# Kernel tuning notes

Hardware: AMD Instinct MI355X
Metric: run time of the kernel (lower is better)

Reference implementation:

```python
import jax, jax.numpy as jnp
import numpy as np

N = 524288
E = 16          # embedding_dim
R = 128         # dense grid resolution
H = 128         # hidden_dim
W0_SIREN = 30.0


def trilinear(grid, p):
    """grid: [R,R,R,E]; p: [N,3] in [0,1]. Returns [N,E]."""
    r = grid.shape[0]
    x = p * (r - 1)
    i0 = jnp.clip(jnp.floor(x), 0, r - 2).astype(jnp.int32)   # [N,3]
    f = x - i0.astype(x.dtype)                                # [N,3] fractional
    gf = grid.reshape(-1, grid.shape[-1])                     # [R^3, E]
    out = jnp.zeros((p.shape[0], grid.shape[-1]), dtype=grid.dtype)
    for dx in (0, 1):
        wx = f[:, 0] if dx else (1.0 - f[:, 0])
        for dy in (0, 1):
            wy = f[:, 1] if dy else (1.0 - f[:, 1])
            for dz in (0, 1):
                wz = f[:, 2] if dz else (1.0 - f[:, 2])
                idx = (i0[:, 0] + dx) * r * r + (i0[:, 1] + dy) * r + (i0[:, 2] + dz)
                out = out + gf[idx] * (wx * wy * wz)[:, None]
    return out


def siren(h, W0, b0, W1, b1, Wo, bo):
    h = jnp.sin(W0_SIREN * (h @ W0.T + b0))
    h = jnp.sin(W0_SIREN * (h @ W1.T + b1))
    return h @ Wo.T + bo   # [N,1]


def setup_inputs() -> dict:
    key = jax.random.key(0)
    ks = jax.random.split(key, 8)
    positions = jax.random.uniform(ks[0], (N, 3), dtype=jnp.float32)  # in [0,1)
    grid = jax.random.uniform(ks[1], (R, R, R, E), jnp.float32, -1e-4, 1e-4)
    din = E + 3
    c0 = float(np.sqrt(6.0 / din) / W0_SIREN)
    c1 = float(np.sqrt(6.0 / H) / W0_SIREN)
    W0 = jax.random.uniform(ks[2], (H, din), jnp.float32, -c0, c0)
    b0 = jax.random.uniform(ks[3], (H,), jnp.float32, -c0, c0)
    W1 = jax.random.uniform(ks[4], (H, H), jnp.float32, -c1, c1)
    b1 = jax.random.uniform(ks[5], (H,), jnp.float32, -c1, c1)
    Wo = jax.random.uniform(ks[6], (1, H), jnp.float32, -c1, c1)
    bo = jax.random.uniform(ks[7], (1,), jnp.float32, -c1, c1)
    return {"positions": positions, "grid": grid, "W0": W0, "b0": b0,
            "W1": W1, "b1": b1, "Wo": Wo, "bo": bo}


def reference(positions, grid, W0, b0, W1, b1, Wo, bo):
    # torch code rebinds positions = positions*0.5+0.5 BEFORE autograd.grad,
    # so the eikonal gradient is w.r.t. the transformed coordinates p.
    p = positions * 0.5 + 0.5

    def sdf_fn(pp):
        emb = trilinear(grid, pp)
        return siren(jnp.concatenate([emb, pp], axis=-1), W0, b0, W1, b1, Wo, bo)

    sdf, vjp_fn = jax.vjp(sdf_fn, p)
    (grad_x,) = vjp_fn(jnp.ones_like(sdf))
    return sdf, grad_x
```

## Files before the change

kernel.cpp:

```cpp
#include <hip/hip_runtime.h>
#include <math.h>

#define NPTS 524288
#define EDIM 16
#define RES  128
#define HDIM 128
#define DIN  19
#define OXs  (RES*RES*EDIM)
#define OYs  (RES*EDIM)
#define OZs  (EDIM)
#define NBLK 256
#define NITER (NPTS / (NBLK * 128))

typedef _Float16 f16;
typedef __attribute__((ext_vector_type(8))) _Float16 f16x8;
typedef __attribute__((ext_vector_type(4))) float f32x4;

#define WS_P1 0
#define WS_P2 32768
#define WS_P0 65536
#define WS_P3 73728
#define WS_T  81920
#define WS_BYTES 84992

__global__ void pack_weights(const float* __restrict__ W0, const float* __restrict__ b0,
                             const float* __restrict__ W1, const float* __restrict__ b1,
                             const float* __restrict__ Wo, unsigned char* __restrict__ ws) {
    int idx = blockIdx.x * 256 + threadIdx.x;
    f16* p1 = (f16*)(ws + WS_P1);
    f16* p2 = (f16*)(ws + WS_P2);
    f16* p0 = (f16*)(ws + WS_P0);
    f16* p3 = (f16*)(ws + WS_P3);
    float* tb = (float*)(ws + WS_T);
    if (idx < 16384) {
        int e = idx & 7, l = (idx >> 3) & 63, t = (idx >> 9) & 3, nt = idx >> 11;
        int c = l & 15, g = l >> 4;
        p1[idx] = (f16)W1[(c + 16*nt)*HDIM + (8*g + e + 32*t)];
    } else if (idx < 32768) {
        int i = idx - 16384;
        int e = i & 7, l = (i >> 3) & 63, t = (i >> 9) & 3, nt = i >> 11;
        int c = l & 15, g = l >> 4;
        p2[i] = (f16)W1[(8*g + e + 32*t)*HDIM + (c + 16*nt)];
    } else if (idx < 36864) {
        int i = idx - 32768;
        int e = i & 7, l = (i >> 3) & 63, nt = i >> 9;
        int c = l & 15, g = l >> 4;
        int d = 8*g + e;
        p0[i] = (d < EDIM) ? (f16)W0[(c + 16*nt)*DIN + d] : (f16)0.f;
    } else if (idx < 40960) {
        int i = idx - 36864;
        int e = i & 7, l = (i >> 3) & 63, t = (i >> 9) & 3, nt = i >> 11;
        int c = l & 15, g = l >> 4;
        int din = c + 16*nt;
        p3[i] = (din < DIN) ? (f16)W0[(8*g + e + 32*t)*DIN + din] : (f16)0.f;
    } else if (idx < 41728) {
        int i = idx - 40960;
        int j = i & 127, sel = i >> 7;
        float v;
        if (sel == 0)      v = W0[j*DIN + 16];
        else if (sel == 1) v = W0[j*DIN + 17];
        else if (sel == 2) v = W0[j*DIN + 18];
        else if (sel == 3) v = b0[j];
        else if (sel == 4) v = b1[j];
        else               v = Wo[j];
        tb[i] = v;
    }
}

__global__ __launch_bounds__(512, 2)
void sdf_mfma(const float* __restrict__ pos,
              const float* __restrict__ gridp,
              const unsigned char* __restrict__ ws,
              const float* __restrict__ bo,
              float* __restrict__ out) {
    __shared__ f16 sP1[16384];
    __shared__ f16 sP2[16384];
    __shared__ f16 sP0[4096];
    __shared__ f16 sP3[4096];
    __shared__ float sT[768];
    __shared__ unsigned char sBounce[8][4352];

    const int tid = threadIdx.x;
    {
        const uint4* src = (const uint4*)ws;
        uint4* d1 = (uint4*)sP1;
        uint4* d2 = (uint4*)sP2;
        uint4* d0 = (uint4*)sP0;
        uint4* d3 = (uint4*)sP3;
        uint4* dt = (uint4*)sT;
        d1[tid]        = src[tid];
        d1[tid + 512]  = src[tid + 512];
        d1[tid + 1024] = src[tid + 1024];
        d1[tid + 1536] = src[tid + 1536];
        d2[tid]        = src[2048 + tid];
        d2[tid + 512]  = src[2560 + tid];
        d2[tid + 1024] = src[3072 + tid];
        d2[tid + 1536] = src[3584 + tid];
        d0[tid] = src[4096 + tid];
        d3[tid] = src[4608 + tid];
        if (tid < 192) dt[tid] = src[5120 + tid];
    }
    __syncthreads();

    const int l = tid & 63, w = tid >> 6;
    const int c = l & 15, g = l >> 4;

    f16* sBW = (f16*)sBounce[w];
    const f16x8* P0 = (const f16x8*)sP0;
    const f16x8* P1 = (const f16x8*)sP1;
    const f16x8* P2 = (const f16x8*)sP2;
    const f16x8* P3 = (const f16x8*)sP3;
    const f32x4 z4 = {0.f, 0.f, 0.f, 0.f};
    const float bov = bo[0];

#pragma unroll 1
    for (int it = 0; it < NITER; ++it) {
        const int pbase = (blockIdx.x * NITER + it) * 128 + w * 16;
        const int pt = pbase + c;

        const float px = fmaf(pos[3*pt+0], 0.5f, 0.5f);
        const float py = fmaf(pos[3*pt+1], 0.5f, 0.5f);
        const float pz = fmaf(pos[3*pt+2], 0.5f, 0.5f);
        const float x0 = px*127.f, x1 = py*127.f, x2 = pz*127.f;
        int i0 = (int)floorf(x0); i0 = i0 < 0 ? 0 : (i0 > 126 ? 126 : i0);
        int i1 = (int)floorf(x1); i1 = i1 < 0 ? 0 : (i1 > 126 ? 126 : i1);
        int i2 = (int)floorf(x2); i2 = i2 < 0 ? 0 : (i2 > 126 ? 126 : i2);
        const float f0 = x0 - (float)i0, f1 = x1 - (float)i1, f2 = x2 - (float)i2;
        const float wx1 = f0, wx0 = 1.f - f0;
        const float wy1 = f1, wy0 = 1.f - f1;
        const float wz1 = f2, wz0 = 1.f - f2;
        const float* gb = gridp + (size_t)((i0*RES + i1)*RES + i2)*EDIM;

        float w8[8] = {0.f,0.f,0.f,0.f,0.f,0.f,0.f,0.f};
        if (g < 2) {
#pragma unroll
            for (int cr = 0; cr < 8; ++cr) {
                const float* gp = gb + ((cr>>2)&1)*OXs + ((cr>>1)&1)*OYs + (cr&1)*OZs + 8*g;
                float4 qa = *(const float4*)gp;
                float4 qb = *(const float4*)(gp + 4);
                const float wc = ((cr&4)?wx1:wx0) * ((cr&2)?wy1:wy0) * ((cr&1)?wz1:wz0);
                w8[0] = fmaf(wc, qa.x, w8[0]);  w8[1] = fmaf(wc, qa.y, w8[1]);
                w8[2] = fmaf(wc, qa.z, w8[2]);  w8[3] = fmaf(wc, qa.w, w8[3]);
                w8[4] = fmaf(wc, qb.x, w8[4]);  w8[5] = fmaf(wc, qb.y, w8[5]);
                w8[6] = fmaf(wc, qb.z, w8[6]);  w8[7] = fmaf(wc, qb.w, w8[7]);
            }
        }
        f16x8 afe;
#pragma unroll
        for (int m = 0; m < 8; ++m) afe[m] = (f16)w8[m];

        f32x4 acc[8];
#pragma unroll
        for (int nt = 0; nt < 8; ++nt)
            acc[nt] = __builtin_amdgcn_mfma_f32_16x16x32_f16(afe, P0[nt*64 + l], z4, 0, 0, 0);

        float rpx[4], rpy[4], rpz[4];
#pragma unroll
        for (int r = 0; r < 4; ++r) {
            const int pr = pbase + 4*g + r;
            rpx[r] = fmaf(pos[3*pr+0], 0.5f, 0.5f);
            rpy[r] = fmaf(pos[3*pr+1], 0.5f, 0.5f);
            rpz[r] = fmaf(pos[3*pr+2], 0.5f, 0.5f);
        }
        float t0a[8][4];
#pragma unroll
        for (int nt = 0; nt < 8; ++nt) {
            const int j = c + 16*nt;
            const float t16 = sT[j], t17 = sT[128+j], t18 = sT[256+j], tb0 = sT[384+j];
#pragma unroll
            for (int r = 0; r < 4; ++r) {
                float a0 = acc[nt][r] + tb0;
                a0 = fmaf(rpx[r], t16, a0);
                a0 = fmaf(rpy[r], t17, a0);
                a0 = fmaf(rpz[r], t18, a0);
                const float t0 = 30.f * a0;
                t0a[nt][r] = t0;
                sBW[(4*g + r)*136 + j] = (f16)__sinf(t0);
            }
        }
        asm volatile("s_waitcnt lgkmcnt(0)" ::: "memory");

        f16x8 af[4];
#pragma unroll
        for (int t = 0; t < 4; ++t)
            af[t] = *(const f16x8*)&sBW[c*136 + 32*t + 8*g];
#pragma unroll
        for (int nt = 0; nt < 8; ++nt) {
            f32x4 a = z4;
#pragma unroll
            for (int t = 0; t < 4; ++t)
                a = __builtin_amdgcn_mfma_f32_16x16x32_f16(af[t], P1[(nt*4+t)*64 + l], a, 0, 0, 0);
            acc[nt] = a;
        }

        float sp[4] = {0.f, 0.f, 0.f, 0.f};
#pragma unroll
        for (int nt = 0; nt < 8; ++nt) {
            const int j = c + 16*nt;
            const float b1j = sT[512+j], woj = sT[640+j];
#pragma unroll
            for (int r = 0; r < 4; ++r) {
                const float t1 = 30.f * (acc[nt][r] + b1j);
                sp[r] = fmaf(woj, __sinf(t1), sp[r]);
                sBW[(4*g + r)*136 + j] = (f16)(30.f * woj * __cosf(t1));
            }
        }
#pragma unroll
        for (int r = 0; r < 4; ++r) {
            sp[r] += __shfl_xor(sp[r], 1);
            sp[r] += __shfl_xor(sp[r], 2);
            sp[r] += __shfl_xor(sp[r], 4);
            sp[r] += __shfl_xor(sp[r], 8);
        }
        if (c == 0) {
#pragma unroll
            for (int r = 0; r < 4; ++r) out[pbase + 4*g + r] = sp[r] + bov;
        }
        asm volatile("s_waitcnt lgkmcnt(0)" ::: "memory");

        float4 ca[2][4];
#pragma unroll
        for (int h = 0; h < 2; ++h) {
            const int cr = 2*g + h;
            const float* gp = gb + ((cr>>2)&1)*OXs + ((cr>>1)&1)*OYs + (cr&1)*OZs;
            ca[h][0] = *(const float4*)gp;
            ca[h][1] = *(const float4*)(gp + 4);
            ca[h][2] = *(const float4*)(gp + 8);
            ca[h][3] = *(const float4*)(gp + 12);
        }

#pragma unroll
        for (int t = 0; t < 4; ++t)
            af[t] = *(const f16x8*)&sBW[c*136 + 32*t + 8*g];
#pragma unroll
        for (int nt = 0; nt < 8; ++nt) {
            f32x4 a = z4;
#pragma unroll
            for (int t = 0; t < 4; ++t)
                a = __builtin_amdgcn_mfma_f32_16x16x32_f16(af[t], P2[(nt*4+t)*64 + l], a, 0, 0, 0);
            acc[nt] = a;
        }

#pragma unroll
        for (int nt = 0; nt < 8; ++nt) {
            const int k = c + 16*nt;
#pragma unroll
            for (int r = 0; r < 4; ++r) {
                const float da0 = acc[nt][r] * (30.f * __cosf(t0a[nt][r]));
                sBW[(4*g + r)*136 + k] = (f16)da0;
            }
        }
        asm volatile("s_waitcnt lgkmcnt(0)" ::: "memory");

#pragma unroll
        for (int t = 0; t < 4; ++t)
            af[t] = *(const f16x8*)&sBW[c*136 + 32*t + 8*g];
        f32x4 d3a = z4, d3b = z4;
#pragma unroll
        for (int t = 0; t < 4; ++t) {
            d3a = __builtin_amdgcn_mfma_f32_16x16x32_f16(af[t], P3[t*64 + l],     d3a, 0, 0, 0);
            d3b = __builtin_amdgcn_mfma_f32_16x16x32_f16(af[t], P3[(4+t)*64 + l], d3b, 0, 0, 0);
        }

        float* sDV = (float*)sBounce[w];
#pragma unroll
        for (int r = 0; r < 4; ++r) sDV[(4*g + r)*20 + c] = d3a[r];
        if (c < 3) {
#pragma unroll
            for (int r = 0; r < 4; ++r) sDV[(4*g + r)*20 + 16 + c] = d3b[r];
        }
        asm volatile("s_waitcnt lgkmcnt(0)" ::: "memory");

        const f32x4 dva = *(const f32x4*)&sDV[c*20 + 0];
        const f32x4 dvb = *(const f32x4*)&sDV[c*20 + 4];
        const f32x4 dvc = *(const f32x4*)&sDV[c*20 + 8];
        const f32x4 dvd = *(const f32x4*)&sDV[c*20 + 12];
        float scv[2];
#pragma unroll
        for (int h = 0; h < 2; ++h) {
            float s = ca[h][0].x*dva[0] + ca[h][0].y*dva[1] + ca[h][0].z*dva[2] + ca[h][0].w*dva[3]
                    + ca[h][1].x*dvb[0] + ca[h][1].y*dvb[1] + ca[h][1].z*dvb[2] + ca[h][1].w*dvb[3]
                    + ca[h][2].x*dvc[0] + ca[h][2].y*dvc[1] + ca[h][2].z*dvc[2] + ca[h][2].w*dvc[3]
                    + ca[h][3].x*dvd[0] + ca[h][3].y*dvd[1] + ca[h][3].z*dvd[2] + ca[h][3].w*dvd[3];
            scv[h] = s;
        }
        float* sSC = (float*)sBounce[w] + 320;
        sSC[c*8 + 2*g]     = scv[0];
        sSC[c*8 + 2*g + 1] = scv[1];
        asm volatile("s_waitcnt lgkmcnt(0)" ::: "memory");
        if (g == 0) {
            const float* scp = &sSC[c*8];
            const float sc0 = scp[0], sc1 = scp[1], sc2 = scp[2], sc3 = scp[3];
            const float sc4 = scp[4], sc5 = scp[5], sc6 = scp[6], sc7 = scp[7];
            const float gx = 127.f * (wy0*wz0*(sc4-sc0) + wy0*wz1*(sc5-sc1) +
                                      wy1*wz0*(sc6-sc2) + wy1*wz1*(sc7-sc3));
            const float gy = 127.f * (wx0*wz0*(sc2-sc0) + wx0*wz1*(sc3-sc1) +
                                      wx1*wz0*(sc6-sc4) + wx1*wz1*(sc7-sc5));
            const float gz = 127.f * (wx0*wy0*(sc1-sc0) + wx0*wy1*(sc3-sc2) +
                                      wx1*wy0*(sc5-sc4) + wx1*wy1*(sc7-sc6));
            out[NPTS + 3*pt + 0] = gx + sDV[c*20 + 16];
            out[NPTS + 3*pt + 1] = gy + sDV[c*20 + 17];
            out[NPTS + 3*pt + 2] = gz + sDV[c*20 + 18];
        }
    }
}

#define JCHUNK 64
__global__ void transpose_w1(const float* __restrict__ W1, float* __restrict__ W1T) {
    int idx = blockIdx.x * 256 + threadIdx.x;
    if (idx < HDIM * HDIM) {
        int j = idx >> 7, k = idx & 127;
        W1T[k * HDIM + j] = W1[j * HDIM + k];
    }
}
#define LOAD16(gq)                                   \
    float4 q0 = *(const float4*)((gq) + 0);          \
    float4 q1 = *(const float4*)((gq) + 4);          \
    float4 q2 = *(const float4*)((gq) + 8);          \
    float4 q3 = *(const float4*)((gq) + 12);

template<int RS, int CS>
__global__ __launch_bounds__(256, 2)
void sdf_fused(const float* __restrict__ pos, const float* __restrict__ gridp,
               const float* __restrict__ W0, const float* __restrict__ b0,
               const float* __restrict__ W1m, const float* __restrict__ b1,
               const float* __restrict__ Wo, const float* __restrict__ bo,
               float* __restrict__ out) {
    const int i = blockIdx.x * 256 + threadIdx.x;
    if (i >= NPTS) return;
    const float W0S = 30.0f;
    const float px = fmaf(pos[3*i+0], 0.5f, 0.5f);
    const float py = fmaf(pos[3*i+1], 0.5f, 0.5f);
    const float pz = fmaf(pos[3*i+2], 0.5f, 0.5f);
    const float x0 = px*127.f, x1 = py*127.f, x2 = pz*127.f;
    int i0 = (int)floorf(x0); i0 = i0 < 0 ? 0 : (i0 > 126 ? 126 : i0);
    int i1 = (int)floorf(x1); i1 = i1 < 0 ? 0 : (i1 > 126 ? 126 : i1);
    int i2 = (int)floorf(x2); i2 = i2 < 0 ? 0 : (i2 > 126 ? 126 : i2);
    const float f0 = x0-(float)i0, f1 = x1-(float)i1, f2 = x2-(float)i2;
    const float wx1 = f0, wx0 = 1.f-f0, wy1 = f1, wy0 = 1.f-f1, wz1 = f2, wz0 = 1.f-f2;
    const float* gb = gridp + (size_t)((i0*RES+i1)*RES+i2)*EDIM;
    float cw[8];
    cw[0]=wx0*wy0*wz0; cw[1]=wx0*wy0*wz1; cw[2]=wx0*wy1*wz0; cw[3]=wx0*wy1*wz1;
    cw[4]=wx1*wy0*wz0; cw[5]=wx1*wy0*wz1; cw[6]=wx1*wy1*wz0; cw[7]=wx1*wy1*wz1;
    float v[DIN];
#pragma unroll
    for (int e = 0; e < EDIM; ++e) v[e] = 0.f;
#pragma unroll
    for (int cr = 0; cr < 8; ++cr) {
        const float* gq = gb + ((cr>>2)&1)*OXs + ((cr>>1)&1)*OYs + (cr&1)*OZs;
        LOAD16(gq);
        const float wc = cw[cr];
        v[0]=fmaf(wc,q0.x,v[0]); v[1]=fmaf(wc,q0.y,v[1]); v[2]=fmaf(wc,q0.z,v[2]); v[3]=fmaf(wc,q0.w,v[3]);
        v[4]=fmaf(wc,q1.x,v[4]); v[5]=fmaf(wc,q1.y,v[5]); v[6]=fmaf(wc,q1.z,v[6]); v[7]=fmaf(wc,q1.w,v[7]);
        v[8]=fmaf(wc,q2.x,v[8]); v[9]=fmaf(wc,q2.y,v[9]); v[10]=fmaf(wc,q2.z,v[10]); v[11]=fmaf(wc,q2.w,v[11]);
        v[12]=fmaf(wc,q3.x,v[12]); v[13]=fmaf(wc,q3.y,v[13]); v[14]=fmaf(wc,q3.z,v[14]); v[15]=fmaf(wc,q3.w,v[15]);
    }
    v[16]=px; v[17]=py; v[18]=pz;
    float dv[DIN];
#pragma unroll
    for (int m = 0; m < DIN; ++m) dv[m] = 0.f;
    float sdf = bo[0];
#pragma unroll 1
    for (int cch = 0; cch < HDIM/JCHUNK; ++cch) {
        const int j0 = cch * JCHUNK;
        float a1c[JCHUNK];
#pragma unroll
        for (int jj = 0; jj < JCHUNK; ++jj) a1c[jj] = 0.f;
#pragma unroll 1
        for (int k = 0; k < HDIM; ++k) {
            float a0 = b0[k];
            const float* w0r = W0 + k*DIN;
#pragma unroll
            for (int m = 0; m < DIN; ++m) a0 = fmaf(w0r[m], v[m], a0);
            const float h1 = __sinf(W0S*a0);
            const float* wr = W1m + k*RS + j0*CS;
#pragma unroll
            for (int jj = 0; jj < JCHUNK; ++jj) a1c[jj] = fmaf(wr[jj*CS], h1, a1c[jj]);
        }
#pragma unroll
        for (int jj = 0; jj < JCHUNK; ++jj) {
            const float t = W0S*(a1c[jj] + b1[j0+jj]);
            float s, co; __sincosf(t, &s, &co);
            const float wo = Wo[j0+jj];
            sdf = fmaf(wo, s, sdf);
            a1c[jj] = (W0S*wo)*co;
        }
#pragma unroll 1
        for (int k = 0; k < HDIM; ++k) {
            const float* wr = W1m + k*RS + j0*CS;
            float s0=0.f,s1=0.f,s2=0.f,s3=0.f;
#pragma unroll
            for (int jj = 0; jj < JCHUNK; jj += 4) {
                s0 = fmaf(wr[(jj+0)*CS], a1c[jj+0], s0);
                s1 = fmaf(wr[(jj+1)*CS], a1c[jj+1], s1);
                s2 = fmaf(wr[(jj+2)*CS], a1c[jj+2], s2);
                s3 = fmaf(wr[(jj+3)*CS], a1c[jj+3], s3);
            }
            const float dh1 = (s0+s1)+(s2+s3);
            float a0 = b0[k];
            const float* w0r = W0 + k*DIN;
#pragma unroll
            for (int m = 0; m < DIN; ++m) a0 = fmaf(w0r[m], v[m], a0);
            const float da0 = dh1 * W0S * __cosf(W0S*a0);
#pragma unroll
            for (int m = 0; m < DIN; ++m) dv[m] = fmaf(w0r[m], da0, dv[m]);
        }
    }
    float sc[8];
#pragma unroll
    for (int cr = 0; cr < 8; ++cr) {
        const float* gq = gb + ((cr>>2)&1)*OXs + ((cr>>1)&1)*OYs + (cr&1)*OZs;
        LOAD16(gq);
        float t0 = q0.x*dv[0]+q0.y*dv[1]+q0.z*dv[2]+q0.w*dv[3];
        float t1 = q1.x*dv[4]+q1.y*dv[5]+q1.z*dv[6]+q1.w*dv[7];
        float t2 = q2.x*dv[8]+q2.y*dv[9]+q2.z*dv[10]+q2.w*dv[11];
        float t3 = q3.x*dv[12]+q3.y*dv[13]+q3.z*dv[14]+q3.w*dv[15];
        sc[cr] = (t0+t1)+(t2+t3);
    }
    const float gx = 127.f*(wy0*wz0*(sc[4]-sc[0]) + wy0*wz1*(sc[5]-sc[1]) + wy1*wz0*(sc[6]-sc[2]) + wy1*wz1*(sc[7]-sc[3]));
    const float gy = 127.f*(wx0*wz0*(sc[2]-sc[0]) + wx0*wz1*(sc[3]-sc[1]) + wx1*wz0*(sc[6]-sc[4]) + wx1*wz1*(sc[7]-sc[5]));
    const float gz = 127.f*(wx0*wy0*(sc[1]-sc[0]) + wx0*wy1*(sc[3]-sc[2]) + wx1*wy0*(sc[5]-sc[4]) + wx1*wy1*(sc[7]-sc[6]));
    out[i] = sdf;
    out[NPTS + 3*i + 0] = gx + dv[16];
    out[NPTS + 3*i + 1] = gy + dv[17];
    out[NPTS + 3*i + 2] = gz + dv[18];
}

extern "C" void kernel_launch(void* const* d_in, const int* in_sizes, int n_in,
                              void* d_out, int out_size, void* d_ws, size_t ws_size,
                              hipStream_t stream) {
    const float* pos  = (const float*)d_in[0];
    const float* grid = (const float*)d_in[1];
    const float* W0   = (const float*)d_in[2];
    const float* b0   = (const float*)d_in[3];
    const float* W1   = (const float*)d_in[4];
    const float* b1   = (const float*)d_in[5];
    const float* Wo   = (const float*)d_in[6];
    const float* bo   = (const float*)d_in[7];
    float* out = (float*)d_out;

    if (ws_size >= (size_t)WS_BYTES) {
        pack_weights<<<(41728 + 255)/256, 256, 0, stream>>>(W0, b0, W1, b1, Wo, (unsigned char*)d_ws);
        sdf_mfma<<<NBLK, 512, 0, stream>>>(pos, grid, (const unsigned char*)d_ws, bo, out);
    } else if (ws_size >= (size_t)(HDIM*HDIM*sizeof(float))) {
        float* W1T = (float*)d_ws;
        transpose_w1<<<(HDIM*HDIM + 255)/256, 256, 0, stream>>>(W1, W1T);
        sdf_fused<HDIM, 1><<<NPTS/256, 256, 0, stream>>>(pos, grid, W0, b0, W1T, b1, Wo, bo, out);
    } else {
        sdf_fused<1, HDIM><<<NPTS/256, 256, 0, stream>>>(pos, grid, W0, b0, W1, b1, Wo, bo, out);
    }
}
```

Measured before the change: 123.7 us.

## Process two 16-point batches per wave per iteration to interleave stages

Each wave now handles two independent 16-point tiles per loop iteration, with a separate LDS bounce buffer for each, and runs each stage (embedding+layer0, layer1, backward layer1, backward layer0/grid grads) for both tiles before the next wait. The point is to give the scheduler two independent MFMA/transcendental chains so gather and LDS latency are hidden, and to halve the number of waitcnt barriers per point. In exchange, register pressure rises (t0a doubles to 64 floats) under launch_bounds(512,2), LDS per block roughly doubles for the bounce buffers, and there is a risk of spills or lower occupancy.

```diff
diff --git a/kernel.cpp b/kernel.cpp
--- a/kernel.cpp
+++ b/kernel.cpp
@@ -10,7 +10,7 @@
 #define OYs  (RES*EDIM)
 #define OZs  (EDIM)
 #define NBLK 256
-#define NITER (NPTS / (NBLK * 128))
+#define NITER 8
 
 typedef _Float16 f16;
 typedef __attribute__((ext_vector_type(8))) _Float16 f16x8;
@@ -78,7 +78,7 @@
     __shared__ f16 sP0[4096];
     __shared__ f16 sP3[4096];
     __shared__ float sT[768];
-    __shared__ unsigned char sBounce[8][4352];
+    __shared__ unsigned char sBounce[8][2][4352];
 
     const int tid = threadIdx.x;
     {
@@ -105,7 +105,8 @@
     const int l = tid & 63, w = tid >> 6;
     const int c = l & 15, g = l >> 4;
 
-    f16* sBW = (f16*)sBounce[w];
+    f16* const sBW0 = (f16*)sBounce[w][0];
+    f16* const sBW1 = (f16*)sBounce[w][1];
     const f16x8* P0 = (const f16x8*)sP0;
     const f16x8* P1 = (const f16x8*)sP1;
     const f16x8* P2 = (const f16x8*)sP2;
@@ -115,192 +116,222 @@
 
 #pragma unroll 1
     for (int it = 0; it < NITER; ++it) {
-        const int pbase = (blockIdx.x * NITER + it) * 128 + w * 16;
-        const int pt = pbase + c;
-
-        const float px = fmaf(pos[3*pt+0], 0.5f, 0.5f);
-        const float py = fmaf(pos[3*pt+1], 0.5f, 0.5f);
-        const float pz = fmaf(pos[3*pt+2], 0.5f, 0.5f);
-        const float x0 = px*127.f, x1 = py*127.f, x2 = pz*127.f;
-        int i0 = (int)floorf(x0); i0 = i0 < 0 ? 0 : (i0 > 126 ? 126 : i0);
-        int i1 = (int)floorf(x1); i1 = i1 < 0 ? 0 : (i1 > 126 ? 126 : i1);
-        int i2 = (int)floorf(x2); i2 = i2 < 0 ? 0 : (i2 > 126 ? 126 : i2);
-        const float f0 = x0 - (float)i0, f1 = x1 - (float)i1, f2 = x2 - (float)i2;
-        const float wx1 = f0, wx0 = 1.f - f0;
-        const float wy1 = f1, wy0 = 1.f - f1;
-        const float wz1 = f2, wz0 = 1.f - f2;
-        const float* gb = gridp + (size_t)((i0*RES + i1)*RES + i2)*EDIM;
-
-        float w8[8] = {0.f,0.f,0.f,0.f,0.f,0.f,0.f,0.f};
-        if (g < 2) {
-#pragma unroll
-            for (int cr = 0; cr < 8; ++cr) {
-                const float* gp = gb + ((cr>>2)&1)*OXs + ((cr>>1)&1)*OYs + (cr&1)*OZs + 8*g;
-                float4 qa = *(const float4*)gp;
-                float4 qb = *(const float4*)(gp + 4);
-                const float wc = ((cr&4)?wx1:wx0) * ((cr&2)?wy1:wy0) * ((cr&1)?wz1:wz0);
-                w8[0] = fmaf(wc, qa.x, w8[0]);  w8[1] = fmaf(wc, qa.y, w8[1]);
-                w8[2] = fmaf(wc, qa.z, w8[2]);  w8[3] = fmaf(wc, qa.w, w8[3]);
-                w8[4] = fmaf(wc, qb.x, w8[4]);  w8[5] = fmaf(wc, qb.y, w8[5]);
-                w8[6] = fmaf(wc, qb.z, w8[6]);  w8[7] = fmaf(wc, qb.w, w8[7]);
-            }
-        }
-        f16x8 afe;
-#pragma unroll
-        for (int m = 0; m < 8; ++m) afe[m] = (f16)w8[m];
-
-        f32x4 acc[8];
-#pragma unroll
-        for (int nt = 0; nt < 8; ++nt)
-            acc[nt] = __builtin_amdgcn_mfma_f32_16x16x32_f16(afe, P0[nt*64 + l], z4, 0, 0, 0);
-
-        float rpx[4], rpy[4], rpz[4];
-#pragma unroll
-        for (int r = 0; r < 4; ++r) {
-            const int pr = pbase + 4*g + r;
-            rpx[r] = fmaf(pos[3*pr+0], 0.5f, 0.5f);
-            rpy[r] = fmaf(pos[3*pr+1], 0.5f, 0.5f);
-            rpz[r] = fmaf(pos[3*pr+2], 0.5f, 0.5f);
-        }
-        float t0a[8][4];
-#pragma unroll
-        for (int nt = 0; nt < 8; ++nt) {
-            const int j = c + 16*nt;
-            const float t16 = sT[j], t17 = sT[128+j], t18 = sT[256+j], tb0 = sT[384+j];
+        const int base = (blockIdx.x * NITER + it) * 256 + w * 32;
+
+        float t0a[2][8][4];
+        const float* gb[2];
+        float wx0[2], wx1[2], wy0[2], wy1[2], wz0[2], wz1[2];
+
+#pragma unroll
+        for (int b = 0; b < 2; ++b) {
+            f16* const sBW = b ? sBW1 : sBW0;
+            const int pbase = base + b * 16;
+            const int pt = pbase + c;
+
+            const float px = fmaf(pos[3*pt+0], 0.5f, 0.5f);
+            const float py = fmaf(pos[3*pt+1], 0.5f, 0.5f);
+            const float pz = fmaf(pos[3*pt+2], 0.5f, 0.5f);
+            const float x0 = px*127.f, x1 = py*127.f, x2 = pz*127.f;
+            int i0 = (int)floorf(x0); i0 = i0 < 0 ? 0 : (i0 > 126 ? 126 : i0);
+            int i1 = (int)floorf(x1); i1 = i1 < 0 ? 0 : (i1 > 126 ? 126 : i1);
+            int i2 = (int)floorf(x2); i2 = i2 < 0 ? 0 : (i2 > 126 ? 126 : i2);
+            const float f0 = x0 - (float)i0, f1 = x1 - (float)i1, f2 = x2 - (float)i2;
+            wx1[b] = f0; wx0[b] = 1.f - f0;
+            wy1[b] = f1; wy0[b] = 1.f - f1;
+            wz1[b] = f2; wz0[b] = 1.f - f2;
+            gb[b] = gridp + (size_t)((i0*RES + i1)*RES + i2)*EDIM;
+
+            float w8[8] = {0.f,0.f,0.f,0.f,0.f,0.f,0.f,0.f};
+            if (g < 2) {
+#pragma unroll
+                for (int cr = 0; cr < 8; ++cr) {
+                    const float* gp = gb[b] + ((cr>>2)&1)*OXs + ((cr>>1)&1)*OYs + (cr&1)*OZs + 8*g;
+                    float4 qa = *(const float4*)gp;
+                    float4 qb = *(const float4*)(gp + 4);
+                    const float wc = ((cr&4)?wx1[b]:wx0[b]) * ((cr&2)?wy1[b]:wy0[b]) * ((cr&1)?wz1[b]:wz0[b]);
+                    w8[0] = fmaf(wc, qa.x, w8[0]);  w8[1] = fmaf(wc, qa.y, w8[1]);
+                    w8[2] = fmaf(wc, qa.z, w8[2]);  w8[3] = fmaf(wc, qa.w, w8[3]);
+                    w8[4] = fmaf(wc, qb.x, w8[4]);  w8[5] = fmaf(wc, qb.y, w8[5]);
+                    w8[6] = fmaf(wc, qb.z, w8[6]);  w8[7] = fmaf(wc, qb.w, w8[7]);
+                }
+            }
+            f16x8 afe;
+#pragma unroll
+            for (int m = 0; m < 8; ++m) afe[m] = (f16)w8[m];
+
+            f32x4 acc[8];
+#pragma unroll
+            for (int nt = 0; nt < 8; ++nt)
+                acc[nt] = __builtin_amdgcn_mfma_f32_16x16x32_f16(afe, P0[nt*64 + l], z4, 0, 0, 0);
+
+            float rpx[4], rpy[4], rpz[4];
 #pragma unroll
             for (int r = 0; r < 4; ++r) {
-                float a0 = acc[nt][r] + tb0;
-                a0 = fmaf(rpx[r], t16, a0);
-                a0 = fmaf(rpy[r], t17, a0);
-                a0 = fmaf(rpz[r], t18, a0);
-                const float t0 = 30.f * a0;
-                t0a[nt][r] = t0;
-                sBW[(4*g + r)*136 + j] = (f16)__sinf(t0);
+                const int pr = pbase + 4*g + r;
+                rpx[r] = fmaf(pos[3*pr+0], 0.5f, 0.5f);
+                rpy[r] = fmaf(pos[3*pr+1], 0.5f, 0.5f);
+                rpz[r] = fmaf(pos[3*pr+2], 0.5f, 0.5f);
+            }
+#pragma unroll
+            for (int nt = 0; nt < 8; ++nt) {
+                const int j = c + 16*nt;
+                const float t16 = sT[j], t17 = sT[128+j], t18 = sT[256+j], tb0 = sT[384+j];
+#pragma unroll
+                for (int r = 0; r < 4; ++r) {
+                    float a0 = acc[nt][r] + tb0;
+                    a0 = fmaf(rpx[r], t16, a0);
+                    a0 = fmaf(rpy[r], t17, a0);
+                    a0 = fmaf(rpz[r], t18, a0);
+                    const float t0 = 30.f * a0;
+                    t0a[b][nt][r] = t0;
+                    sBW[(4*g + r)*136 + j] = (f16)__sinf(t0);
+                }
             }
         }
         asm volatile("s_waitcnt lgkmcnt(0)" ::: "memory");
 
-        f16x8 af[4];
-#pragma unroll
-        for (int t = 0; t < 4; ++t)
-            af[t] = *(const f16x8*)&sBW[c*136 + 32*t + 8*g];
-#pragma unroll
-        for (int nt = 0; nt < 8; ++nt) {
-            f32x4 a = z4;
+#pragma unroll
+        for (int b = 0; b < 2; ++b) {
+            f16* const sBW = b ? sBW1 : sBW0;
+            const int pbase = base + b * 16;
+
+            f16x8 af[4];
 #pragma unroll
             for (int t = 0; t < 4; ++t)
-                a = __builtin_amdgcn_mfma_f32_16x16x32_f16(af[t], P1[(nt*4+t)*64 + l], a, 0, 0, 0);
-            acc[nt] = a;
-        }
-
-        float sp[4] = {0.f, 0.f, 0.f, 0.f};
-#pragma unroll
-        for (int nt = 0; nt < 8; ++nt) {
-            const int j = c + 16*nt;
-            const float b1j = sT[512+j], woj = sT[640+j];
+                af[t] = *(const f16x8*)&sBW[c*136 + 32*t + 8*g];
+            f32x4 acc[8];
+#pragma unroll
+            for (int nt = 0; nt < 8; ++nt) {
+                f32x4 a = z4;
+#pragma unroll
+                for (int t = 0; t < 4; ++t)
+                    a = __builtin_amdgcn_mfma_f32_16x16x32_f16(af[t], P1[(nt*4+t)*64 + l], a, 0, 0, 0);
+                acc[nt] = a;
+            }
+
+            float sp[4] = {0.f, 0.f, 0.f, 0.f};
+#pragma unroll
+            for (int nt = 0; nt < 8; ++nt) {
+                const int j = c + 16*nt;
+                const float b1j = sT[512+j], woj = sT[640+j];
+#pragma unroll
+                for (int r = 0; r < 4; ++r) {
+                    const float t1 = 30.f * (acc[nt][r] + b1j);
+                    sp[r] = fmaf(woj, __sinf(t1), sp[r]);
+                    sBW[(4*g + r)*136 + j] = (f16)(30.f * woj * __cosf(t1));
+                }
+            }
 #pragma unroll
             for (int r = 0; r < 4; ++r) {
-                const float t1 = 30.f * (acc[nt][r] + b1j);
-                sp[r] = fmaf(woj, __sinf(t1), sp[r]);
-                sBW[(4*g + r)*136 + j] = (f16)(30.f * woj * __cosf(t1));
-            }
-        }
-#pragma unroll
-        for (int r = 0; r < 4; ++r) {
-            sp[r] += __shfl_xor(sp[r], 1);
-            sp[r] += __shfl_xor(sp[r], 2);
-            sp[r] += __shfl_xor(sp[r], 4);
-            sp[r] += __shfl_xor(sp[r], 8);
-        }
-        if (c == 0) {
-#pragma unroll
-            for (int r = 0; r < 4; ++r) out[pbase + 4*g + r] = sp[r] + bov;
+                sp[r] += __shfl_xor(sp[r], 1);
+                sp[r] += __shfl_xor(sp[r], 2);
+                sp[r] += __shfl_xor(sp[r], 4);
+                sp[r] += __shfl_xor(sp[r], 8);
+            }
+            if (c == 0) {
+#pragma unroll
+                for (int r = 0; r < 4; ++r) out[pbase + 4*g + r] = sp[r] + bov;
+            }
         }
         asm volatile("s_waitcnt lgkmcnt(0)" ::: "memory");
 
-        float4 ca[2][4];
-#pragma unroll
-        for (int h = 0; h < 2; ++h) {
-            const int cr = 2*g + h;
-            const float* gp = gb + ((cr>>2)&1)*OXs + ((cr>>1)&1)*OYs + (cr&1)*OZs;
-            ca[h][0] = *(const float4*)gp;
-            ca[h][1] = *(const float4*)(gp + 4);
-            ca[h][2] = *(const float4*)(gp + 8);
-            ca[h][3] = *(const float4*)(gp + 12);
-        }
-
-#pragma unroll
-        for (int t = 0; t < 4; ++t)
-            af[t] = *(const f16x8*)&sBW[c*136 + 32*t + 8*g];
-#pragma unroll
-        for (int nt = 0; nt < 8; ++nt) {
-            f32x4 a = z4;
+#pragma unroll
+        for (int b = 0; b < 2; ++b) {
+            f16* const sBW = b ? sBW1 : sBW0;
+
+            f16x8 af[4];
 #pragma unroll
             for (int t = 0; t < 4; ++t)
-                a = __builtin_amdgcn_mfma_f32_16x16x32_f16(af[t], P2[(nt*4+t)*64 + l], a, 0, 0, 0);
-            acc[nt] = a;
-        }
-
-#pragma unroll
-        for (int nt = 0; nt < 8; ++nt) {
-            const int k = c + 16*nt;
-#pragma unroll
-            for (int r = 0; r < 4; ++r) {
-                const float da0 = acc[nt][r] * (30.f * __cosf(t0a[nt][r]));
-                sBW[(4*g + r)*136 + k] = (f16)da0;
+                af[t] = *(const f16x8*)&sBW[c*136 + 32*t + 8*g];
+            f32x4 acc[8];
+#pragma unroll
+            for (int nt = 0; nt < 8; ++nt) {
+                f32x4 a = z4;
+#pragma unroll
+                for (int t = 0; t < 4; ++t)
+                    a = __builtin_amdgcn_mfma_f32_16x16x32_f16(af[t], P2[(nt*4+t)*64 + l], a, 0, 0, 0);
+                acc[nt] = a;
+            }
+#pragma unroll
+            for (int nt = 0; nt < 8; ++nt) {
+                const int k = c + 16*nt;
+#pragma unroll
+                for (int r = 0; r < 4; ++r) {
+                    const float da0 = acc[nt][r] * (30.f * __cosf(t0a[b][nt][r]));
+                    sBW[(4*g + r)*136 + k] = (f16)da0;
+                }
             }
         }
         asm volatile("s_waitcnt lgkmcnt(0)" ::: "memory");
 
 #pragma unroll
-        for (int t = 0; t < 4; ++t)
-            af[t] = *(const f16x8*)&sBW[c*136 + 32*t + 8*g];
-        f32x4 d3a = z4, d3b = z4;
-#pragma unroll
-        for (int t = 0; t < 4; ++t) {
-            d3a = __builtin_amdgcn_mfma_f32_16x16x32_f16(af[t], P3[t*64 + l],     d3a, 0, 0, 0);
-            d3b = __builtin_amdgcn_mfma_f32_16x16x32_f16(af[t], P3[(4+t)*64 + l], d3b, 0, 0, 0);
-        }
-
-        float* sDV = (float*)sBounce[w];
-#pragma unroll
-        for (int r = 0; r < 4; ++r) sDV[(4*g + r)*20 + c] = d3a[r];
-        if (c < 3) {
-#pragma unroll
-            for (int r = 0; r < 4; ++r) sDV[(4*g + r)*20 + 16 + c] = d3b[r];
-        }
-        asm volatile("s_waitcnt lgkmcnt(0)" ::: "memory");
-
-        const f32x4 dva = *(const f32x4*)&sDV[c*20 + 0];
-        const f32x4 dvb = *(const f32x4*)&sDV[c*20 + 4];
-        const f32x4 dvc = *(const f32x4*)&sDV[c*20 + 8];
-        const f32x4 dvd = *(const f32x4*)&sDV[c*20 + 12];
-        float scv[2];
-#pragma unroll
-        for (int h = 0; h < 2; ++h) {
-            float s = ca[h][0].x*dva[0] + ca[h][0].y*dva[1] + ca[h][0].z*dva[2] + ca[h][0].w*dva[3]
-                    + ca[h][1].x*dvb[0] + ca[h][1].y*dvb[1] + ca[h][1].z*dvb[2] + ca[h][1].w*dvb[3]
-                    + ca[h][2].x*dvc[0] + ca[h][2].y*dvc[1] + ca[h][2].z*dvc[2] + ca[h][2].w*dvc[3]
-                    + ca[h][3].x*dvd[0] + ca[h][3].y*dvd[1] + ca[h][3].z*dvd[2] + ca[h][3].w*dvd[3];
-            scv[h] = s;
-        }
-        float* sSC = (float*)sBounce[w] + 320;
-        sSC[c*8 + 2*g]     = scv[0];
-        sSC[c*8 + 2*g + 1] = scv[1];
-        asm volatile("s_waitcnt lgkmcnt(0)" ::: "memory");
-        if (g == 0) {
-            const float* scp = &sSC[c*8];
-            const float sc0 = scp[0], sc1 = scp[1], sc2 = scp[2], sc3 = scp[3];
-            const float sc4 = scp[4], sc5 = scp[5], sc6 = scp[6], sc7 = scp[7];
-            const float gx = 127.f * (wy0*wz0*(sc4-sc0) + wy0*wz1*(sc5-sc1) +
-                                      wy1*wz0*(sc6-sc2) + wy1*wz1*(sc7-sc3));
-            const float gy = 127.f * (wx0*wz0*(sc2-sc0) + wx0*wz1*(sc3-sc1) +
-                                      wx1*wz0*(sc6-sc4) + wx1*wz1*(sc7-sc5));
-            const float gz = 127.f * (wx0*wy0*(sc1-sc0) + wx0*wy1*(sc3-sc2) +
-                                      wx1*wy0*(sc5-sc4) + wx1*wy1*(sc7-sc6));
-            out[NPTS + 3*pt + 0] = gx + sDV[c*20 + 16];
-            out[NPTS + 3*pt + 1] = gy + sDV[c*20 + 17];
-            out[NPTS + 3*pt + 2] = gz + sDV[c*20 + 18];
+        for (int b = 0; b < 2; ++b) {
+            f16* const sBW = b ? sBW1 : sBW0;
+            const int pbase = base + b * 16;
+            const int pt = pbase + c;
+
+            float4 ca[2][4];
+#pragma unroll
+            for (int h = 0; h < 2; ++h) {
+                const int cr = 2*g + h;
+                const float* gp = gb[b] + ((cr>>2)&1)*OXs + ((cr>>1)&1)*OYs + (cr&1)*OZs;
+                ca[h][0] = *(const float4*)gp;
+                ca[h][1] = *(const float4*)(gp + 4);
+                ca[h][2] = *(const float4*)(gp + 8);
+                ca[h][3] = *(const float4*)(gp + 12);
+            }
+
+            f16x8 af[4];
+#pragma unroll
+            for (int t = 0; t < 4; ++t)
+                af[t] = *(const f16x8*)&sBW[c*136 + 32*t + 8*g];
+            f32x4 d3a = z4, d3b = z4;
+#pragma unroll
+            for (int t = 0; t < 4; ++t) {
+                d3a = __builtin_amdgcn_mfma_f32_16x16x32_f16(af[t], P3[t*64 + l],     d3a, 0, 0, 0);
+                d3b = __builtin_amdgcn_mfma_f32_16x16x32_f16(af[t], P3[(4+t)*64 + l], d3b, 0, 0, 0);
+            }
+
+            float* sDV = (float*)sBW;
+#pragma unroll
+            for (int r = 0; r < 4; ++r) sDV[(4*g + r)*20 + c] = d3a[r];
+            if (c < 3) {
+#pragma unroll
+                for (int r = 0; r < 4; ++r) sDV[(4*g + r)*20 + 16 + c] = d3b[r];
+            }
+            asm volatile("s_waitcnt lgkmcnt(0)" ::: "memory");
+
+            const f32x4 dva = *(const f32x4*)&sDV[c*20 + 0];
+            const f32x4 dvb = *(const f32x4*)&sDV[c*20 + 4];
+            const f32x4 dvc = *(const f32x4*)&sDV[c*20 + 8];
+            const f32x4 dvd = *(const f32x4*)&sDV[c*20 + 12];
+            float scv[2];
+#pragma unroll
+            for (int h = 0; h < 2; ++h) {
+                float s = ca[h][0].x*dva[0] + ca[h][0].y*dva[1] + ca[h][0].z*dva[2] + ca[h][0].w*dva[3]
+                        + ca[h][1].x*dvb[0] + ca[h][1].y*dvb[1] + ca[h][1].z*dvb[2] + ca[h][1].w*dvb[3]
+                        + ca[h][2].x*dvc[0] + ca[h][2].y*dvc[1] + ca[h][2].z*dvc[2] + ca[h][2].w*dvc[3]
+                        + ca[h][3].x*dvd[0] + ca[h][3].y*dvd[1] + ca[h][3].z*dvd[2] + ca[h][3].w*dvd[3];
+                scv[h] = s;
+            }
+            float* sSC = (float*)sBW + 320;
+            sSC[c*8 + 2*g]     = scv[0];
+            sSC[c*8 + 2*g + 1] = scv[1];
+            asm volatile("s_waitcnt lgkmcnt(0)" ::: "memory");
+            if (g == 0) {
+                const float* scp = &sSC[c*8];
+                const float sc0 = scp[0], sc1 = scp[1], sc2 = scp[2], sc3 = scp[3];
+                const float sc4 = scp[4], sc5 = scp[5], sc6 = scp[6], sc7 = scp[7];
+                const float gx = 127.f * (wy0[b]*wz0[b]*(sc4-sc0) + wy0[b]*wz1[b]*(sc5-sc1) +
+                                          wy1[b]*wz0[b]*(sc6-sc2) + wy1[b]*wz1[b]*(sc7-sc3));
+                const float gy = 127.f * (wx0[b]*wz0[b]*(sc2-sc0) + wx0[b]*wz1[b]*(sc3-sc1) +
+                                          wx1[b]*wz0[b]*(sc6-sc4) + wx1[b]*wz1[b]*(sc7-sc5));
+                const float gz = 127.f * (wx0[b]*wy0[b]*(sc1-sc0) + wx0[b]*wy1[b]*(sc3-sc2) +
+                                          wx1[b]*wy0[b]*(sc5-sc4) + wx1[b]*wy1[b]*(sc7-sc6));
+                out[NPTS + 3*pt + 0] = gx + sDV[c*20 + 16];
+                out[NPTS + 3*pt + 1] = gy + sDV[c*20 + 17];
+                out[NPTS + 3*pt + 2] = gz + sDV[c*20 + 18];
+            }
         }
     }
 }
```

New measurement: 135.3 us. +9.4%, slower.
